# Performance work log

Measured on AMD Instinct MI355X. Metric: run time of the kernel, lower is better.

The kernel has to match this reference:

```python
import jax, jax.numpy as jnp
import numpy as np

N_Q = 10           # qubits
N_BLOCKS = 10      # encoding blocks (== N_Q so adjoint start-index arithmetic matches source)
DIM = 1 << N_Q     # 1024 state-vector dimension
P = 128            # number of data points -> P*P pairwise circuit evaluations

SQRT2 = np.float32(np.sqrt(2.0))

# bits[d, q] = q-th bit (MSB-first) of basis index d
_bits_np = ((np.arange(DIM)[:, None] >> (N_Q - 1 - np.arange(N_Q))) & 1).astype(np.float32)
BITS = jnp.asarray(_bits_np)  # [DIM, N_Q]
# CRZ-ring diagonal feature: control q, target (q+1) % N_Q; phase exp(1j*theta_q*s_q*(s_{q+1}-1/2))
RING = jnp.asarray(_bits_np * (np.roll(_bits_np, -1, axis=1) - 0.5))  # [DIM, N_Q]


def _apply_1q(state, U, q):
    # state: [B, DIM]; apply 2x2 U to qubit q (MSB-first ordering)
    B = state.shape[0]
    s = state.reshape(B, 1 << q, 2, 1 << (N_Q - q - 1))
    s = jnp.einsum('ij,bajc->baic', U, s)
    return s.reshape(B, DIM)


def h_layer(state):
    H = jnp.asarray([[1, 1], [1, -1]], dtype=state.dtype) / SQRT2
    for q in range(N_Q):
        state = _apply_1q(state, H, q)
    return state


def rz_layer(state, thetas):
    # thetas: [B, N_Q] per-pair data angles; RZ(t) = diag(e^{-it/2}, e^{it/2})
    phases = jnp.exp(1j * jnp.einsum('dq,bq->bd', BITS - 0.5, thetas))
    return state * phases.astype(state.dtype)


def ry_layer(state, thetas):
    # thetas: [N_Q] shared trainable angles
    for q in range(N_Q):
        c, s = jnp.cos(thetas[q] / 2), jnp.sin(thetas[q] / 2)
        U = jnp.stack([jnp.stack([c, -s]), jnp.stack([s, c])]).astype(state.dtype)
        state = _apply_1q(state, U, q)
    return state


def crz_ring(state, thetas):
    # entire CRZ ring is diagonal in the computational basis -> single fused multiply
    phases = jnp.exp(1j * (RING @ thetas))  # [DIM]
    return state * phases.astype(state.dtype)


def circuit(x1, x2, params):
    # x1, x2: [B, N_BLOCKS*N_Q]; params: [N_BLOCKS, 2, N_Q]
    B = x1.shape[0]
    state = jnp.zeros((B, DIM), jnp.complex64).at[:, 0].set(1.0)
    for j in range(N_BLOCKS):  # block(...)
        state = h_layer(state)
        state = rz_layer(state, x1[:, j * N_Q:(j + 1) * N_Q])
        state = ry_layer(state, params[j, 0])
        state = crz_ring(state, params[j, 1])
    for k in range(N_BLOCKS):  # adj_block(...) over reversed(params)
        bp = params[N_BLOCKS - 1 - k]
        start = (N_Q - k - 1) * N_Q  # exactly as written in the source
        state = crz_ring(state, -bp[1])   # adjoint of diagonal gate = negated angles
        state = ry_layer(state, -bp[0])   # RY(-t); single-qubit gates commute across qubits
        state = rz_layer(state, -x2[:, start:start + N_Q])
        state = h_layer(state)            # H is self-adjoint
    return state


def setup_inputs() -> dict:
    key = jax.random.key(0)
    k1, k2, k3 = jax.random.split(key, 3)
    data = jax.random.normal(k1, (P, N_BLOCKS * N_Q), jnp.float32)
    labels = jnp.sign(jax.random.normal(k2, (P,), jnp.float32))  # +/-1 class labels
    params = jax.random.normal(k3, (N_BLOCKS, 2, N_Q), jnp.float32)
    return {"data": data, "labels": labels, "params": params}


def reference(data, labels, params):
    # k_fusion: kernel-target-alignment over all (i, j) pairs, fully batched
    n = data.shape[0]
    x1 = jnp.repeat(data, n, axis=0)   # point i for each pair (pair-major)
    x2 = jnp.tile(data, (n, 1))        # point j for each pair
    state = circuit(x1, x2, params)
    K = (jnp.abs(state[:, 0]) ** 2).reshape(n, n)  # probability of |0...0>
    ll = labels[:, None] * labels[None, :]
    polarity = jnp.sum(ll * K)
    norm = jnp.sqrt(jnp.sum(K ** 2) * jnp.sum(ll ** 2))
    return polarity / norm
```

## Files before the change

### kernel.cpp

```cpp
#include <hip/hip_runtime.h>
#include <math.h>

#define NQ   10
#define DIM  1024
#define NB   10
#define NPTS 128
#define S2   0.70710678118654752440f

#define TS 32
#define KC 64
#define KSPLIT (DIM / KC)
#define NBLK_RED 64

typedef float f2 __attribute__((ext_vector_type(2)));

__device__ __forceinline__ f2 cmul(f2 a, f2 b) {
    return (f2){a.x * b.x - a.y * b.y, a.x * b.y + a.y * b.x};
}

__global__ __launch_bounds__(64)
void states_kernel(const float* __restrict__ data,
                   const float* __restrict__ params,
                   float2* __restrict__ psi,
                   double* __restrict__ acc,
                   int* __restrict__ cnt)
{
    __shared__ f2    T[16 * 65];
    __shared__ f2    UT[NB * NQ * 4];
    __shared__ f2    Lt[NB * 64];
    __shared__ f2    Gt[NB * 64];
    __shared__ float sCrz[NB * NQ];

    const int lane = threadIdx.x;
    const int pt   = blockIdx.x;

    if (pt == 0 && lane == 0) { acc[0] = 0.0; acc[1] = 0.0; cnt[0] = 0; }

    for (int e = lane; e < NB * NQ; e += 64) {
        const int j = e / NQ, q = e - j * NQ;
        float c, s;
        __sincosf(0.5f * params[j * 2 * NQ + q], &s, &c);
        float cx, sx;
        __sincosf(0.5f * data[pt * (NB * NQ) + e], &sx, &cx);
        const float al = (c - s) * S2, be = (c + s) * S2;
        f2* u = &UT[e * 4];
        u[0] = (f2){ al * cx, -be * sx};
        u[1] = (f2){ be * cx, -al * sx};
        u[2] = (f2){ be * cx,  al * sx};
        u[3] = (f2){-al * cx, -be * sx};
        sCrz[e] = params[j * 2 * NQ + NQ + q];
    }
    for (int e = lane; e < NB * 64; e += 64) {
        const int j = e >> 6, r = e & 63;
        const float* phi = &sCrz[j * NQ];
        const float r0 = (float)(r & 1),        r1 = (float)((r >> 1) & 1);
        const float r2 = (float)((r >> 2) & 1), r3 = (float)((r >> 3) & 1);
        const float r4 = (float)((r >> 4) & 1), r5 = (float)((r >> 5) & 1);
        const float m0 = r2, m1 = r3, m2 = r4, m3 = r5;
        const float bA = r1, bB = r0;
        float L, G;
        if ((j & 1) == 0) {
            L = phi[4] * r5 * (r4 - 0.5f) + phi[5] * r4 * (r3 - 0.5f)
              + phi[6] * r3 * (r2 - 0.5f) + phi[7] * r2 * (r1 - 0.5f)
              + phi[8] * r1 * (r0 - 0.5f);
            G = phi[0] * m3 * (m2 - 0.5f) + phi[1] * m2 * (m1 - 0.5f)
              + phi[2] * m1 * (m0 - 0.5f) + phi[3] * m0 * (bA - 0.5f)
              + phi[9] * bB * (m3 - 0.5f);
        } else {
            L = phi[0] * r5 * (r4 - 0.5f) + phi[1] * r4 * (r3 - 0.5f)
              + phi[2] * r3 * (r2 - 0.5f) + phi[3] * r2 * (r1 - 0.5f)
              + phi[4] * r1 * (r0 - 0.5f);
            G = phi[6] * m3 * (m2 - 0.5f) + phi[7] * m2 * (m1 - 0.5f)
              + phi[8] * m1 * (m0 - 0.5f) + phi[5] * bA * (m3 - 0.5f)
              + phi[9] * m0 * (bB - 0.5f);
        }
        float s, c;
        __sincosf(L, &s, &c);  Lt[e] = (f2){c, s};
        __sincosf(G, &s, &c);  Gt[e] = (f2){c, s};
    }

    #define APPLY(j, q, bit) { \
        const f2* _u = &UT[((j) * NQ + (q)) * 4]; \
        const f2 u0 = _u[0], u1 = _u[1], u2 = _u[2], u3 = _u[3]; \
        _Pragma("unroll") \
        for (int m = 0; m < 16; ++m) if (!(m & (bit))) { \
            const f2 a0 = v[m], a1 = v[m | (bit)]; \
            v[m]         = cmul(u0, a0) + cmul(u1, a1); \
            v[m | (bit)] = cmul(u2, a0) + cmul(u3, a1); \
        } }

    #define TWRITE() { \
        _Pragma("unroll") \
        for (int m = 0; m < 16; ++m) T[m * 65 + lane] = v[m]; }

    #define READ_AD() { \
        const int base = 65 * (lane & 15) + ((lane >> 4) << 4); \
        _Pragma("unroll") \
        for (int m = 0; m < 16; ++m) v[m] = T[base + m]; }

    #define READ_B() { \
        _Pragma("unroll") \
        for (int m = 0; m < 16; ++m) \
            v[m] = T[65 * (((m & 3) << 2) | (lane >> 4)) + ((m >> 2) << 4) + (lane & 15)]; }

    #define READ_C() { \
        _Pragma("unroll") \
        for (int m = 0; m < 16; ++m) \
            v[m] = T[65 * (((lane >> 4) << 2) | (m >> 2)) + ((m & 3) << 4) + (lane & 15)]; }

    #define CRZ(j, crossIdx) { \
        const f2 l = Lt[((j) << 6) | lane]; \
        _Pragma("unroll") \
        for (int m = 0; m < 16; ++m) { \
            const f2 g = Gt[((j) << 6) | (m << 2) | (crossIdx)]; \
            v[m] = cmul(v[m], cmul(l, g)); \
        } }

    f2 v[16];
    {
        f2 f = cmul(UT[9 * 4 + (lane & 1) * 2],        UT[8 * 4 + ((lane >> 1) & 1) * 2]);
        f = cmul(f, cmul(UT[7 * 4 + ((lane >> 2) & 1) * 2], UT[6 * 4 + ((lane >> 3) & 1) * 2]));
        f = cmul(f, cmul(UT[5 * 4 + ((lane >> 4) & 1) * 2], UT[4 * 4 + ((lane >> 5) & 1) * 2]));
        #pragma unroll
        for (int m = 0; m < 16; ++m) {
            const f2 rm = cmul(cmul(UT[0 * 4 + ((m >> 3) & 1) * 2],
                                    UT[1 * 4 + ((m >> 2) & 1) * 2]),
                               cmul(UT[2 * 4 + ((m >> 1) & 1) * 2],
                                    UT[3 * 4 + (m & 1) * 2]));
            v[m] = cmul(rm, f);
        }
    }
    const int crossEven = (((lane >> 5) & 1) << 1) | (lane & 1);
    const int crossOdd  = ((lane & 1) << 1) | ((lane >> 5) & 1);
    CRZ(0, crossEven)

    #pragma unroll 1
    for (int j = 1; j < NB; ++j) {
        if (j & 1) {
            APPLY(j, 0, 8) APPLY(j, 1, 4) APPLY(j, 2, 2) APPLY(j, 3, 1)
            TWRITE() READ_C()
            APPLY(j, 4, 2) APPLY(j, 5, 1)
            TWRITE() READ_AD()
            APPLY(j, 6, 8) APPLY(j, 7, 4) APPLY(j, 8, 2) APPLY(j, 9, 1)
            CRZ(j, crossOdd)
        } else {
            APPLY(j, 6, 8) APPLY(j, 7, 4) APPLY(j, 8, 2) APPLY(j, 9, 1)
            TWRITE() READ_AD()
            APPLY(j, 2, 8) APPLY(j, 3, 4) APPLY(j, 4, 2) APPLY(j, 5, 1)
            TWRITE() READ_B()
            APPLY(j, 0, 8) APPLY(j, 1, 4)
            CRZ(j, crossEven)
        }
    }

    float2* o = psi + (size_t)pt * DIM + lane * 16;
    #pragma unroll
    for (int k = 0; k < 8; ++k)
        *(float4*)&o[2 * k] = make_float4(v[2*k].x, v[2*k].y, v[2*k+1].x, v[2*k+1].y);
}

__global__ __launch_bounds__(256)
void gram_kernel(const float2* __restrict__ psi, float2* __restrict__ Gpart)
{
    __shared__ float2 A [TS][KC + 2];
    __shared__ float2 Bt[KC][TS + 2];

    const int tid  = threadIdx.x;
    const int bx   = blockIdx.x;
    const int ks   = bx & 15;
    const int tile = bx >> 4;
    const int ti   = tile >> 2, tj = tile & 3;
    const int kbase = ks * KC;

    #pragma unroll
    for (int it = 0; it < 2; ++it) {
        const int slot = it * 256 + tid;
        const int row  = slot >> 4;
        const int kq   = (slot & 15) << 2;
        const float4* sa = (const float4*)(psi + (ti * TS + row) * DIM + kbase + kq);
        const float4 a01 = sa[0], a23 = sa[1];
        *(float4*)&A[row][kq]     = a01;
        *(float4*)&A[row][kq + 2] = a23;
        const float4* sb = (const float4*)(psi + (tj * TS + row) * DIM + kbase + kq);
        const float4 b01 = sb[0], b23 = sb[1];
        Bt[kq + 0][row] = make_float2(b01.x, b01.y);
        Bt[kq + 1][row] = make_float2(b01.z, b01.w);
        Bt[kq + 2][row] = make_float2(b23.x, b23.y);
        Bt[kq + 3][row] = make_float2(b23.z, b23.w);
    }
    __syncthreads();

    const int ty = tid >> 4, tx = tid & 15;
    float g00r = 0.f, g00i = 0.f, g01r = 0.f, g01i = 0.f;
    float g10r = 0.f, g10i = 0.f, g11r = 0.f, g11i = 0.f;

    #pragma unroll 4
    for (int k = 0; k < KC; k += 2) {
        const float4 a0 = *(const float4*)&A[2 * ty    ][k];
        const float4 a1 = *(const float4*)&A[2 * ty + 1][k];
        const float4 b0 = *(const float4*)&Bt[k    ][2 * tx];
        const float4 b1 = *(const float4*)&Bt[k + 1][2 * tx];
        g00r += a0.x * b0.x + a0.y * b0.y;  g00i += a0.x * b0.y - a0.y * b0.x;
        g01r += a0.x * b0.z + a0.y * b0.w;  g01i += a0.x * b0.w - a0.y * b0.z;
        g10r += a1.x * b0.x + a1.y * b0.y;  g10i += a1.x * b0.y - a1.y * b0.x;
        g11r += a1.x * b0.z + a1.y * b0.w;  g11i += a1.x * b0.w - a1.y * b0.z;
        g00r += a0.z * b1.x + a0.w * b1.y;  g00i += a0.z * b1.y - a0.w * b1.x;
        g01r += a0.z * b1.z + a0.w * b1.w;  g01i += a0.z * b1.w - a0.w * b1.z;
        g10r += a1.z * b1.x + a1.w * b1.y;  g10i += a1.z * b1.y - a1.w * b1.x;
        g11r += a1.z * b1.z + a1.w * b1.w;  g11i += a1.z * b1.w - a1.w * b1.z;
    }

    float2* gp = Gpart + ks * (NPTS * NPTS);
    const int gr0 = ti * TS + 2 * ty, gc0 = tj * TS + 2 * tx;
    gp[(gr0    ) * NPTS + gc0    ] = make_float2(g00r, g00i);
    gp[(gr0    ) * NPTS + gc0 + 1] = make_float2(g01r, g01i);
    gp[(gr0 + 1) * NPTS + gc0    ] = make_float2(g10r, g10i);
    gp[(gr0 + 1) * NPTS + gc0 + 1] = make_float2(g11r, g11i);
}

__global__ __launch_bounds__(256)
void reduce_final(const float2* __restrict__ Gpart,
                  const float* __restrict__ labels,
                  double* __restrict__ acc,
                  int* __restrict__ cnt,
                  float* __restrict__ out)
{
    const int idx = blockIdx.x * 256 + threadIdx.x;
    float gr = 0.f, gi = 0.f;
    #pragma unroll
    for (int p = 0; p < KSPLIT; ++p) {
        const float2 g = Gpart[p * (NPTS * NPTS) + idx];
        gr += g.x; gi += g.y;
    }
    const int i  = idx >> 7;
    const int jj = idx & (NPTS - 1);
    const float K = gr * gr + gi * gi;
    double pol = (double)(labels[i] * labels[jj]) * (double)K;
    double k2  = (double)K * (double)K;
    #pragma unroll
    for (int off = 1; off < 64; off <<= 1) {
        pol += __shfl_xor(pol, off, 64);
        k2  += __shfl_xor(k2,  off, 64);
    }
    __shared__ double sp[4], sk[4];
    const int wv = threadIdx.x >> 6;
    if ((threadIdx.x & 63) == 0) { sp[wv] = pol; sk[wv] = k2; }
    __syncthreads();
    if (threadIdx.x == 0) {
        atomicAdd(&acc[0], sp[0] + sp[1] + sp[2] + sp[3]);
        atomicAdd(&acc[1], sk[0] + sk[1] + sk[2] + sk[3]);
        __threadfence();
        const int done = atomicAdd(cnt, 1);
        if (done == NBLK_RED - 1) {
            const double p  = atomicAdd(&acc[0], 0.0);
            const double s2 = atomicAdd(&acc[1], 0.0);
            double sumL2 = 0.0;
            for (int t = 0; t < NPTS; ++t) {
                const double l = (double)labels[t];
                sumL2 += l * l;
            }
            out[0] = (float)(p / (sumL2 * sqrt(s2)));
        }
    }
}

extern "C" void kernel_launch(void* const* d_in, const int* in_sizes, int n_in,
                              void* d_out, int out_size, void* d_ws, size_t ws_size,
                              hipStream_t stream)
{
    const float* data   = (const float*)d_in[0];
    const float* labels = (const float*)d_in[1];
    const float* params = (const float*)d_in[2];
    float* out = (float*)d_out;

    float2* psi   = (float2*)d_ws;
    float2* Gpart = (float2*)((char*)d_ws + (size_t)(1u << 20));
    double* acc   = (double*)((char*)d_ws + (size_t)(3u << 20));
    int*    cnt   = (int*)   ((char*)d_ws + (size_t)(3u << 20) + 16);

    states_kernel<<<NPTS, 64, 0, stream>>>(data, params, psi, acc, cnt);
    gram_kernel<<<256, 256, 0, stream>>>(psi, Gpart);
    reduce_final<<<NBLK_RED, 64 * 4, 0, stream>>>(Gpart, labels, acc, cnt, out);
}
```

Before: 106.3 us.

## Spread per-point state simulation over 256 threads with 4 amplitudes each

The state-vector kernel moves from one 64-lane wave holding 16 amplitudes per lane to a 256-thread block holding 4 amplitudes per thread. Qubit pairs are applied in registers and a double-buffered shared-memory transpose with block-wide barriers runs between each pair, and the CRZ phase tables are rebuilt to match the new index split. This is meant to raise parallelism, since only 128 blocks of one wave were launched before. The cost is more transposes and __syncthreads per block, plus extra shared-memory traffic.

```diff
diff --git a/kernel.cpp b/kernel.cpp
--- a/kernel.cpp
+++ b/kernel.cpp
@@ -18,145 +18,161 @@
     return (f2){a.x * b.x - a.y * b.y, a.x * b.y + a.y * b.x};
 }
 
-__global__ __launch_bounds__(64)
+__global__ __launch_bounds__(256)
 void states_kernel(const float* __restrict__ data,
                    const float* __restrict__ params,
                    float2* __restrict__ psi,
                    double* __restrict__ acc,
                    int* __restrict__ cnt)
 {
-    __shared__ f2    T[16 * 65];
+    __shared__ f2    Tb[2][1088];
     __shared__ f2    UT[NB * NQ * 4];
-    __shared__ f2    Lt[NB * 64];
-    __shared__ f2    Gt[NB * 64];
+    __shared__ f2    Lt[NB * 256];
+    __shared__ f2    Gt[NB * 16];
     __shared__ float sCrz[NB * NQ];
 
-    const int lane = threadIdx.x;
-    const int pt   = blockIdx.x;
-
-    if (pt == 0 && lane == 0) { acc[0] = 0.0; acc[1] = 0.0; cnt[0] = 0; }
-
-    for (int e = lane; e < NB * NQ; e += 64) {
-        const int j = e / NQ, q = e - j * NQ;
+    const int t  = threadIdx.x;
+    const int pt = blockIdx.x;
+
+    if (pt == 0 && t == 0) { acc[0] = 0.0; acc[1] = 0.0; cnt[0] = 0; }
+
+    if (t < NB * NQ) {
+        const int j = t / NQ, q = t - j * NQ;
         float c, s;
         __sincosf(0.5f * params[j * 2 * NQ + q], &s, &c);
         float cx, sx;
-        __sincosf(0.5f * data[pt * (NB * NQ) + e], &sx, &cx);
+        __sincosf(0.5f * data[pt * (NB * NQ) + t], &sx, &cx);
         const float al = (c - s) * S2, be = (c + s) * S2;
-        f2* u = &UT[e * 4];
+        f2* u = &UT[t * 4];
         u[0] = (f2){ al * cx, -be * sx};
         u[1] = (f2){ be * cx, -al * sx};
         u[2] = (f2){ be * cx,  al * sx};
         u[3] = (f2){-al * cx, -be * sx};
-        sCrz[e] = params[j * 2 * NQ + NQ + q];
-    }
-    for (int e = lane; e < NB * 64; e += 64) {
-        const int j = e >> 6, r = e & 63;
+        sCrz[t] = params[j * 2 * NQ + NQ + q];
+    }
+    __syncthreads();
+
+    if (t < NB * 16) {
+        const int j = t >> 4, r = t & 15;
+        const float m1 = (float)((r >> 3) & 1), m0 = (float)((r >> 2) & 1);
+        const float bA = (float)((r >> 1) & 1), bB = (float)(r & 1);
         const float* phi = &sCrz[j * NQ];
-        const float r0 = (float)(r & 1),        r1 = (float)((r >> 1) & 1);
-        const float r2 = (float)((r >> 2) & 1), r3 = (float)((r >> 3) & 1);
-        const float r4 = (float)((r >> 4) & 1), r5 = (float)((r >> 5) & 1);
-        const float m0 = r2, m1 = r3, m2 = r4, m3 = r5;
-        const float bA = r1, bB = r0;
-        float L, G;
+        float G;
+        if ((j & 1) == 0)
+            G = phi[0] * m1 * (m0 - 0.5f) + phi[1] * m0 * (bA - 0.5f)
+              + phi[9] * bB * (m1 - 0.5f);
+        else
+            G = phi[7] * bB * (m1 - 0.5f) + phi[8] * m1 * (m0 - 0.5f)
+              + phi[9] * m0 * (bA - 0.5f);
+        float s, c;
+        __sincosf(G, &s, &c);
+        Gt[t] = (f2){c, s};
+    }
+    #pragma unroll 1
+    for (int j = 0; j < NB; ++j) {
+        const float* phi = &sCrz[j * NQ];
+        float L = 0.f;
         if ((j & 1) == 0) {
-            L = phi[4] * r5 * (r4 - 0.5f) + phi[5] * r4 * (r3 - 0.5f)
-              + phi[6] * r3 * (r2 - 0.5f) + phi[7] * r2 * (r1 - 0.5f)
-              + phi[8] * r1 * (r0 - 0.5f);
-            G = phi[0] * m3 * (m2 - 0.5f) + phi[1] * m2 * (m1 - 0.5f)
-              + phi[2] * m1 * (m0 - 0.5f) + phi[3] * m0 * (bA - 0.5f)
-              + phi[9] * bB * (m3 - 0.5f);
+            #pragma unroll
+            for (int q = 2; q <= 8; ++q) {
+                const float sq  = (float)((t >> (9 - q)) & 1);
+                const float sq1 = (float)((t >> (8 - q)) & 1);
+                L += phi[q] * sq * (sq1 - 0.5f);
+            }
         } else {
-            L = phi[0] * r5 * (r4 - 0.5f) + phi[1] * r4 * (r3 - 0.5f)
-              + phi[2] * r3 * (r2 - 0.5f) + phi[3] * r2 * (r1 - 0.5f)
-              + phi[4] * r1 * (r0 - 0.5f);
-            G = phi[6] * m3 * (m2 - 0.5f) + phi[7] * m2 * (m1 - 0.5f)
-              + phi[8] * m1 * (m0 - 0.5f) + phi[5] * bA * (m3 - 0.5f)
-              + phi[9] * m0 * (bB - 0.5f);
+            #pragma unroll
+            for (int q = 0; q <= 6; ++q) {
+                const float sq  = (float)((t >> (7 - q)) & 1);
+                const float sq1 = (float)((t >> (6 - q)) & 1);
+                L += phi[q] * sq * (sq1 - 0.5f);
+            }
         }
         float s, c;
-        __sincosf(L, &s, &c);  Lt[e] = (f2){c, s};
-        __sincosf(G, &s, &c);  Gt[e] = (f2){c, s};
-    }
+        __sincosf(L, &s, &c);
+        Lt[j * 256 + t] = (f2){c, s};
+    }
+    __syncthreads();
+
+    int idx[5][4];
+    #pragma unroll
+    for (int k = 0; k < 5; ++k) {
+        #pragma unroll
+        for (int m = 0; m < 4; ++m) {
+            const int lo = t & ((1 << (2 * k)) - 1);
+            const int d  = lo | (m << (2 * k)) | ((t >> (2 * k)) << (2 * k + 2));
+            idx[k][m] = d + (d >> 4);
+        }
+    }
+    const int crossIdx = (((t >> 7) & 1) << 1) | (t & 1);
 
     #define APPLY(j, q, bit) { \
         const f2* _u = &UT[((j) * NQ + (q)) * 4]; \
         const f2 u0 = _u[0], u1 = _u[1], u2 = _u[2], u3 = _u[3]; \
         _Pragma("unroll") \
-        for (int m = 0; m < 16; ++m) if (!(m & (bit))) { \
+        for (int m = 0; m < 4; ++m) if (!(m & (bit))) { \
             const f2 a0 = v[m], a1 = v[m | (bit)]; \
             v[m]         = cmul(u0, a0) + cmul(u1, a1); \
             v[m | (bit)] = cmul(u2, a0) + cmul(u3, a1); \
         } }
 
-    #define TWRITE() { \
+    #define TRANS(kF, kT, B) { \
         _Pragma("unroll") \
-        for (int m = 0; m < 16; ++m) T[m * 65 + lane] = v[m]; }
-
-    #define READ_AD() { \
-        const int base = 65 * (lane & 15) + ((lane >> 4) << 4); \
+        for (int m = 0; m < 4; ++m) Tb[B][idx[kF][m]] = v[m]; \
+        __syncthreads(); \
         _Pragma("unroll") \
-        for (int m = 0; m < 16; ++m) v[m] = T[base + m]; }
-
-    #define READ_B() { \
+        for (int m = 0; m < 4; ++m) v[m] = Tb[B][idx[kT][m]]; }
+
+    #define CRZ(j) { \
+        const f2 l = Lt[(j) * 256 + t]; \
         _Pragma("unroll") \
-        for (int m = 0; m < 16; ++m) \
-            v[m] = T[65 * (((m & 3) << 2) | (lane >> 4)) + ((m >> 2) << 4) + (lane & 15)]; }
-
-    #define READ_C() { \
-        _Pragma("unroll") \
-        for (int m = 0; m < 16; ++m) \
-            v[m] = T[65 * (((lane >> 4) << 2) | (m >> 2)) + ((m & 3) << 4) + (lane & 15)]; }
-
-    #define CRZ(j, crossIdx) { \
-        const f2 l = Lt[((j) << 6) | lane]; \
-        _Pragma("unroll") \
-        for (int m = 0; m < 16; ++m) { \
-            const f2 g = Gt[((j) << 6) | (m << 2) | (crossIdx)]; \
+        for (int m = 0; m < 4; ++m) { \
+            const f2 g = Gt[((j) << 4) | (m << 2) | crossIdx]; \
             v[m] = cmul(v[m], cmul(l, g)); \
         } }
 
-    f2 v[16];
+    f2 v[4];
     {
-        f2 f = cmul(UT[9 * 4 + (lane & 1) * 2],        UT[8 * 4 + ((lane >> 1) & 1) * 2]);
-        f = cmul(f, cmul(UT[7 * 4 + ((lane >> 2) & 1) * 2], UT[6 * 4 + ((lane >> 3) & 1) * 2]));
-        f = cmul(f, cmul(UT[5 * 4 + ((lane >> 4) & 1) * 2], UT[4 * 4 + ((lane >> 5) & 1) * 2]));
+        f2 f = cmul(UT[2 * 4 + ((t >> 7) & 1) * 2], UT[3 * 4 + ((t >> 6) & 1) * 2]);
+        f = cmul(f, cmul(UT[4 * 4 + ((t >> 5) & 1) * 2], UT[5 * 4 + ((t >> 4) & 1) * 2]));
+        f = cmul(f, cmul(UT[6 * 4 + ((t >> 3) & 1) * 2], UT[7 * 4 + ((t >> 2) & 1) * 2]));
+        f = cmul(f, cmul(UT[8 * 4 + ((t >> 1) & 1) * 2], UT[9 * 4 + (t & 1) * 2]));
         #pragma unroll
-        for (int m = 0; m < 16; ++m) {
-            const f2 rm = cmul(cmul(UT[0 * 4 + ((m >> 3) & 1) * 2],
-                                    UT[1 * 4 + ((m >> 2) & 1) * 2]),
-                               cmul(UT[2 * 4 + ((m >> 1) & 1) * 2],
-                                    UT[3 * 4 + (m & 1) * 2]));
-            v[m] = cmul(rm, f);
-        }
-    }
-    const int crossEven = (((lane >> 5) & 1) << 1) | (lane & 1);
-    const int crossOdd  = ((lane & 1) << 1) | ((lane >> 5) & 1);
-    CRZ(0, crossEven)
+        for (int m = 0; m < 4; ++m)
+            v[m] = cmul(cmul(UT[0 * 4 + ((m >> 1) & 1) * 2],
+                             UT[1 * 4 + (m & 1) * 2]), f);
+    }
+    CRZ(0)
 
     #pragma unroll 1
     for (int j = 1; j < NB; ++j) {
         if (j & 1) {
-            APPLY(j, 0, 8) APPLY(j, 1, 4) APPLY(j, 2, 2) APPLY(j, 3, 1)
-            TWRITE() READ_C()
-            APPLY(j, 4, 2) APPLY(j, 5, 1)
-            TWRITE() READ_AD()
-            APPLY(j, 6, 8) APPLY(j, 7, 4) APPLY(j, 8, 2) APPLY(j, 9, 1)
-            CRZ(j, crossOdd)
+            APPLY(j, 1, 1) APPLY(j, 0, 2)
+            TRANS(4, 3, 0)
+            APPLY(j, 3, 1) APPLY(j, 2, 2)
+            TRANS(3, 2, 1)
+            APPLY(j, 5, 1) APPLY(j, 4, 2)
+            TRANS(2, 1, 0)
+            APPLY(j, 7, 1) APPLY(j, 6, 2)
+            TRANS(1, 0, 1)
+            APPLY(j, 9, 1) APPLY(j, 8, 2)
+            CRZ(j)
         } else {
-            APPLY(j, 6, 8) APPLY(j, 7, 4) APPLY(j, 8, 2) APPLY(j, 9, 1)
-            TWRITE() READ_AD()
-            APPLY(j, 2, 8) APPLY(j, 3, 4) APPLY(j, 4, 2) APPLY(j, 5, 1)
-            TWRITE() READ_B()
-            APPLY(j, 0, 8) APPLY(j, 1, 4)
-            CRZ(j, crossEven)
+            APPLY(j, 9, 1) APPLY(j, 8, 2)
+            TRANS(0, 1, 0)
+            APPLY(j, 7, 1) APPLY(j, 6, 2)
+            TRANS(1, 2, 1)
+            APPLY(j, 5, 1) APPLY(j, 4, 2)
+            TRANS(2, 3, 0)
+            APPLY(j, 3, 1) APPLY(j, 2, 2)
+            TRANS(3, 4, 1)
+            APPLY(j, 1, 1) APPLY(j, 0, 2)
+            CRZ(j)
         }
     }
 
-    float2* o = psi + (size_t)pt * DIM + lane * 16;
-    #pragma unroll
-    for (int k = 0; k < 8; ++k)
-        *(float4*)&o[2 * k] = make_float4(v[2*k].x, v[2*k].y, v[2*k+1].x, v[2*k+1].y);
+    float2* o = psi + (size_t)pt * DIM + t * 4;
+    *(float4*)&o[0] = make_float4(v[0].x, v[0].y, v[1].x, v[1].y);
+    *(float4*)&o[2] = make_float4(v[2].x, v[2].y, v[3].x, v[3].y);
 }
 
 __global__ __launch_bounds__(256)
@@ -255,8 +271,8 @@
             const double p  = atomicAdd(&acc[0], 0.0);
             const double s2 = atomicAdd(&acc[1], 0.0);
             double sumL2 = 0.0;
-            for (int t = 0; t < NPTS; ++t) {
-                const double l = (double)labels[t];
+            for (int tt = 0; tt < NPTS; ++tt) {
+                const double l = (double)labels[tt];
                 sumL2 += l * l;
             }
             out[0] = (float)(p / (sumL2 * sqrt(s2)));
@@ -278,7 +294,7 @@
     double* acc   = (double*)((char*)d_ws + (size_t)(3u << 20));
     int*    cnt   = (int*)   ((char*)d_ws + (size_t)(3u << 20) + 16);
 
-    states_kernel<<<NPTS, 64, 0, stream>>>(data, params, psi, acc, cnt);
+    states_kernel<<<NPTS, 256, 0, stream>>>(data, params, psi, acc, cnt);
     gram_kernel<<<256, 256, 0, stream>>>(psi, Gpart);
-    reduce_final<<<NBLK_RED, 64 * 4, 0, stream>>>(Gpart, labels, acc, cnt, out);
-}
+    reduce_final<<<NBLK_RED, 256, 0, stream>>>(Gpart, labels, acc, cnt, out);
+}
```

Result: faster. 86.94 us (-18.2%).
